# Kernel tuning notes

Measured on AMD Instinct MI355X. Metric: run time of the kernel, lower is better.

## Reference

```python
import jax, jax.numpy as jnp
import numpy as np

EMB_DIM = 1024
H = 16
HEAD_DIM = EMB_DIM // H
B = 2
S = 2048  # enc and dec seq len
LN_EPS = 1e-5


def setup_inputs() -> dict:
    key = jax.random.key(0)
    ks = jax.random.split(key, 8)
    scale_in = 1.0 / np.sqrt(EMB_DIM)
    scale_o = 1.0 / np.sqrt(H * HEAD_DIM)
    return {
        "enc_out": jax.random.normal(ks[0], (B, S, EMB_DIM), jnp.float32),
        "dec_out": jax.random.normal(ks[1], (B, S, EMB_DIM), jnp.float32),
        # stacked per-head projections, equivalent to h separate Linear(emb_dim, head_dim, bias=False)
        "Wq": jax.random.uniform(ks[2], (H, EMB_DIM, HEAD_DIM), jnp.float32, -scale_in, scale_in),
        "Wk": jax.random.uniform(ks[3], (H, EMB_DIM, HEAD_DIM), jnp.float32, -scale_in, scale_in),
        "Wv": jax.random.uniform(ks[4], (H, EMB_DIM, HEAD_DIM), jnp.float32, -scale_in, scale_in),
        "Wo": jax.random.uniform(ks[5], (H * HEAD_DIM, EMB_DIM), jnp.float32, -scale_o, scale_o),
        "gamma": jnp.ones((EMB_DIM,), jnp.float32),
        "beta": jnp.zeros((EMB_DIM,), jnp.float32),
    }


def reference(enc_out, dec_out, Wq, Wk, Wv, Wo, gamma, beta):
    d = Wq.shape[-1]
    # per-head projections, batched over heads (same math as the Python loop)
    q = jnp.einsum('bse,hed->bhsd', dec_out, Wq)   # queries from decoder
    k = jnp.einsum('bte,hed->bhtd', enc_out, Wk)   # keys from encoder
    v = jnp.einsum('bte,hed->bhtd', enc_out, Wv)   # values from encoder
    scores = jnp.einsum('bhsd,bhtd->bhst', q, k) / jnp.sqrt(jnp.asarray(d, q.dtype))
    att = jax.nn.softmax(scores, axis=-1)
    ctx = jnp.einsum('bhst,bhtd->bhsd', att, v)
    b, h, s, hd = ctx.shape
    ctx = ctx.transpose(0, 2, 1, 3).reshape(b, s, h * hd)  # concat heads along feature dim
    transformed = ctx @ Wo  # dropout is identity in eval mode
    x = dec_out + transformed
    mu = jnp.mean(x, axis=-1, keepdims=True)
    var = jnp.mean(jnp.square(x - mu), axis=-1, keepdims=True)
    return (x - mu) * jax.lax.rsqrt(var + LN_EPS) * gamma + beta
```

## Files before the change

### kernel.cpp

```cpp
#include <hip/hip_runtime.h>
#include <hip/hip_bf16.h>

#define EMB   1024
#define NH    16
#define HD    64
#define SEQ   2048
#define SA    72

typedef __attribute__((ext_vector_type(8))) short          bf16x8;
typedef __attribute__((ext_vector_type(8))) unsigned short us8;
typedef __attribute__((ext_vector_type(4))) float          f32x4;

__device__ __forceinline__ float u2f(unsigned short u) {
    return __uint_as_float(((unsigned)u) << 16);
}
__device__ __forceinline__ unsigned short f2u(float f) {
    __hip_bfloat16 b = __float2bfloat16(f);
    return *reinterpret_cast<unsigned short*>(&b);
}
__device__ __forceinline__ bool detect_bf16(const void* gamma) {
    return ((const unsigned short*)gamma)[0] == 0x3F80;
}
__device__ __forceinline__ f32x4 fzero() {
    f32x4 v; v.x = v.y = v.z = v.w = 0.f; return v;
}
__device__ __forceinline__ void ld16f(const void* p, size_t idx, bool isbf, float* o) {
    if (isbf) {
        const unsigned short* b = (const unsigned short*)p + idx;
        us8 v0 = *(const us8*)b, v1 = *(const us8*)(b + 8);
        #pragma unroll
        for (int i = 0; i < 8; ++i) { o[i] = u2f(v0[i]); o[8 + i] = u2f(v1[i]); }
    } else {
        const float* f = (const float*)p + idx;
        #pragma unroll
        for (int i = 0; i < 4; ++i) {
            float4 v = *(const float4*)(f + 4 * i);
            o[4*i] = v.x; o[4*i+1] = v.y; o[4*i+2] = v.z; o[4*i+3] = v.w;
        }
    }
}
__device__ __forceinline__ float ld1f(const void* p, size_t i, bool isbf) {
    return isbf ? u2f(((const unsigned short*)p)[i]) : ((const float*)p)[i];
}
__device__ __forceinline__ float4 ld4(const void* p, size_t idx, bool isbf) {
    if (isbf) {
        ushort4 t = *reinterpret_cast<const ushort4*>((const unsigned short*)p + idx);
        return make_float4(u2f(t.x), u2f(t.y), u2f(t.z), u2f(t.w));
    }
    return *reinterpret_cast<const float4*>((const float*)p + idx);
}
__device__ __forceinline__ us8 pk8(const float* s) {
    us8 v;
    #pragma unroll
    for (int i = 0; i < 8; ++i) v[i] = f2u(s[i]);
    return v;
}
__device__ __forceinline__ f32x4 mfma16(bf16x8 a, bf16x8 b, f32x4 c) {
    return __builtin_amdgcn_mfma_f32_16x16x32_bf16(a, b, c, 0, 0, 0);
}
__device__ __forceinline__ bf16x8 mk8(unsigned w0, unsigned w1, unsigned w2, unsigned w3) {
    union { unsigned u[4]; bf16x8 v; } x;
    x.u[0] = w0; x.u[1] = w1; x.u[2] = w2; x.u[3] = w3;
    return x.v;
}
__device__ __forceinline__ void gl_lds16(const unsigned short* g, unsigned short* l) {
    __builtin_amdgcn_global_load_lds(
        (const __attribute__((address_space(1))) void*)g,
        (__attribute__((address_space(3))) void*)l,
        16, 0, 0);
}

#define QSCALE 0.18033688f

__global__ __launch_bounds__(256) void convert_x_kernel(
    const void* __restrict__ dec, const void* __restrict__ enc,
    const void* __restrict__ gamma, unsigned short* __restrict__ xb)
{
    const bool isbf = detect_bf16(gamma);
    const size_t HALF = (size_t)4096 * 1024;
    size_t idx = ((size_t)blockIdx.x * 256 + threadIdx.x) * 16;
    const void* src; size_t off;
    if (idx < HALF) { src = dec; off = idx; } else { src = enc; off = idx - HALF; }
    float buf[16];
    ld16f(src, off, isbf, buf);
    *(us8*)&xb[idx]     = pk8(buf);
    *(us8*)&xb[idx + 8] = pk8(buf + 8);
}

__global__ __launch_bounds__(256) void transpose_w_kernel(
    const void* __restrict__ Wq, const void* __restrict__ Wk,
    const void* __restrict__ Wv, const void* __restrict__ gamma,
    unsigned short* __restrict__ wt)
{
    const bool isbf = detect_bf16(gamma);
    const int which = blockIdx.z, h = blockIdx.y, e0 = blockIdx.x * 64;
    const void* W = (which == 0) ? Wq : (which == 1 ? Wk : Wv);

    __shared__ unsigned short T[64][SA];
    const int sr = threadIdx.x >> 2, sc = (threadIdx.x & 3) * 16;

    float buf[16];
    ld16f(W, ((size_t)h * EMB + e0 + sr) * HD + sc, isbf, buf);
    #pragma unroll
    for (int i = 0; i < 16; ++i) T[sc + i][sr] = f2u(buf[i]);
    __syncthreads();
    us8 v0 = *(const us8*)&T[sr][sc];
    us8 v1 = *(const us8*)&T[sr][sc + 8];
    size_t o = (((size_t)which * NH + h) * HD + sr) * EMB + e0 + sc;
    *(us8*)&wt[o] = v0;
    *(us8*)&wt[o + 8] = v1;
}

__global__ __launch_bounds__(256) void transpose_wo_kernel(
    const void* __restrict__ Wo, const void* __restrict__ gamma,
    unsigned short* __restrict__ wot)
{
    const bool isbf = detect_bf16(gamma);
    const int n0 = blockIdx.x * 64, k0 = blockIdx.y * 64;
    __shared__ unsigned short T[64][SA];
    const int sr = threadIdx.x >> 2, sc = (threadIdx.x & 3) * 16;

    float buf[16];
    ld16f(Wo, (size_t)(k0 + sr) * EMB + n0 + sc, isbf, buf);
    #pragma unroll
    for (int i = 0; i < 16; ++i) T[sc + i][sr] = f2u(buf[i]);
    __syncthreads();
    us8 v0 = *(const us8*)&T[sr][sc];
    us8 v1 = *(const us8*)&T[sr][sc + 8];
    size_t o = (size_t)(n0 + sr) * EMB + k0 + sc;
    *(us8*)&wot[o] = v0;
    *(us8*)&wot[o + 8] = v1;
}

__global__ __launch_bounds__(256) void qkv_kernel(
    const unsigned short* __restrict__ xb,
    const unsigned short* __restrict__ wt,
    unsigned short* __restrict__ qo, unsigned short* __restrict__ ko,
    unsigned short* __restrict__ vt)
{
    const int id = blockIdx.x;
    const int xcd = id & 7, sl = id >> 3;
    const int m_t = xcd * 4 + (sl & 3);
    const int n_t = sl >> 2;
    const int m0 = m_t * 128, n0g = n_t * 128;
    const int which = n0g >> 10;
    const int nloc = n0g & 1023;
    const unsigned short* X = xb + ((which == 0) ? (size_t)0 : (size_t)4096 * 1024);

    __shared__ unsigned short smem[17408];
    unsigned short* const ldsA = smem;
    unsigned short* const ldsB = smem + 8192;

    const int tid = threadIdx.x, wv = tid >> 6, lane = tid & 63;
    const int lq = lane >> 4, lm = lane & 15;
    const int mw = (wv & 1) * 64, nw = (wv >> 1) * 64;

    const unsigned short* Wb = wt + (size_t)(which * 1024 + nloc) * EMB;

    const int seg0 = wv * 4;
    const int srow = lane >> 3;
    const int su   = (lane & 7) ^ srow;
    const unsigned short* aP[4];
    const unsigned short* bP[4];
    #pragma unroll
    for (int q = 0; q < 4; ++q) {
        const int s = seg0 + q;
        aP[q] = X  + (size_t)(m0 + 8 * s + srow) * EMB + su * 8;
        bP[q] = Wb + (size_t)(8 * s + srow) * EMB + su * 8;
    }

    f32x4 acc[4][4];
    #pragma unroll
    for (int i = 0; i < 4; ++i)
        #pragma unroll
        for (int j = 0; j < 4; ++j) acc[i][j] = fzero();

    const int xa = lm & 7;

    for (int k0 = 0; k0 < EMB; k0 += 64) {
        #pragma unroll
        for (int q = 0; q < 4; ++q) {
            gl_lds16(aP[q] + k0, ldsA + (seg0 + q) * 512);
            gl_lds16(bP[q] + k0, ldsB + (seg0 + q) * 512);
        }
        asm volatile("s_waitcnt vmcnt(0)" ::: "memory");
        __syncthreads();

        #pragma unroll
        for (int st = 0; st < 2; ++st) {
            const int u = (st * 4 + lq) ^ xa;
            bf16x8 af[4], bq[4];
            #pragma unroll
            for (int i = 0; i < 4; ++i)
                af[i] = *(const bf16x8*)(ldsA + (mw + i * 16 + lm) * 64 + u * 8);
            #pragma unroll
            for (int j = 0; j < 4; ++j)
                bq[j] = *(const bf16x8*)(ldsB + (nw + j * 16 + lm) * 64 + u * 8);
            #pragma unroll
            for (int i = 0; i < 4; ++i)
                #pragma unroll
                for (int j = 0; j < 4; ++j)
                    acc[i][j] = mfma16(af[i], bq[j], acc[i][j]);
        }
        __syncthreads();
    }

    const int b = m0 >> 11, s0 = m0 & (SEQ - 1);
    const float osc = (which == 0) ? QSCALE : 1.0f;
    if (which != 2) {
        unsigned short* Y = which ? ko : qo;
        #pragma unroll
        for (int i = 0; i < 4; ++i)
            #pragma unroll
            for (int j = 0; j < 4; ++j)
                #pragma unroll
                for (int r = 0; r < 4; ++r) {
                    int m = mw + i * 16 + lq * 4 + r;
                    int n = nloc + nw + j * 16 + lm;
                    int h = n >> 6, d = n & 63;
                    Y[(((size_t)b * NH + h) * SEQ + s0 + m) * HD + d] = f2u(acc[i][j][r] * osc);
                }
    } else {
        __syncthreads();
        unsigned short* vbuf = smem;
        #pragma unroll
        for (int i = 0; i < 4; ++i)
            #pragma unroll
            for (int j = 0; j < 4; ++j) {
                ushort4 p;
                p.x = f2u(acc[i][j][0]); p.y = f2u(acc[i][j][1]);
                p.z = f2u(acc[i][j][2]); p.w = f2u(acc[i][j][3]);
                *(ushort4*)&vbuf[(size_t)(nw + j * 16 + lm) * 136 + mw + i * 16 + lq * 4] = p;
            }
        __syncthreads();
        const int dd = tid >> 1, cc = (tid & 1) * 64;
        const int n = nloc + dd, h = n >> 6, d = n & 63;
        size_t o = (((size_t)b * NH + h) * HD + d) * SEQ + s0 + cc;
        #pragma unroll
        for (int jj = 0; jj < 8; ++jj)
            *(us8*)&vt[o + 8 * jj] = *(const us8*)&vbuf[(size_t)dd * 136 + cc + 8 * jj];
    }
}

__global__ __launch_bounds__(256) void attn_kernel(
    const unsigned short* __restrict__ qg,
    const unsigned short* __restrict__ kg,
    const unsigned short* __restrict__ vtg,
    unsigned short* __restrict__ ctx)
{
    __shared__ unsigned short Ks[2][64][SA];
    __shared__ unsigned short Vt[2][64][SA];

    const int tid = threadIdx.x, wv = tid >> 6, lane = tid & 63;
    const int lq = lane >> 4, lm = lane & 15;
    const int kr = tid >> 2, kc = (tid & 3) * 16;
    const int bh = blockIdx.x, q0 = blockIdx.y * 64;
    const unsigned short* Kg = kg + (size_t)bh * SEQ * HD;
    const unsigned short* Vg = vtg + (size_t)bh * HD * SEQ;

    bf16x8 qf[2];
    #pragma unroll
    for (int st = 0; st < 2; ++st)
        qf[st] = *(const bf16x8*)(qg + (size_t)bh * SEQ * HD
                      + (size_t)(q0 + wv * 16 + lm) * HD + st * 32 + lq * 8);

    bf16x8 onesf;
    #pragma unroll
    for (int i = 0; i < 8; ++i) onesf[i] = (short)0x3F80;

    f32x4 Of[4], lacc = fzero();
    #pragma unroll
    for (int t = 0; t < 4; ++t) Of[t] = fzero();

    us8 kreg0, kreg1, vreg0, vreg1;
    {
        const unsigned short* s1 = Kg + (size_t)kr * HD + kc;
        kreg0 = *(const us8*)s1; kreg1 = *(const us8*)(s1 + 8);
        const unsigned short* s2 = Vg + (size_t)kr * SEQ + kc;
        vreg0 = *(const us8*)s2; vreg1 = *(const us8*)(s2 + 8);
    }

    for (int it = 0; it < SEQ / 64; ++it) {
        const int cur = it & 1;
        *(us8*)&Ks[cur][kr][kc]     = kreg0;
        *(us8*)&Ks[cur][kr][kc + 8] = kreg1;
        *(us8*)&Vt[cur][kr][kc]     = vreg0;
        *(us8*)&Vt[cur][kr][kc + 8] = vreg1;
        __syncthreads();

        if (it + 1 < SEQ / 64) {
            const int t0 = (it + 1) * 64;
            const unsigned short* s1 = Kg + (size_t)(t0 + kr) * HD + kc;
            kreg0 = *(const us8*)s1; kreg1 = *(const us8*)(s1 + 8);
            const unsigned short* s2 = Vg + (size_t)kr * SEQ + t0 + kc;
            vreg0 = *(const us8*)s2; vreg1 = *(const us8*)(s2 + 8);
        }

        f32x4 sf[4];
        #pragma unroll
        for (int t = 0; t < 4; ++t) sf[t] = fzero();
        #pragma unroll
        for (int st = 0; st < 2; ++st)
            #pragma unroll
            for (int tt = 0; tt < 4; ++tt) {
                bf16x8 kf = *(const bf16x8*)&Ks[cur][lm + 16 * tt][st * 32 + lq * 8];
                sf[tt] = mfma16(kf, qf[st], sf[tt]);
            }

        unsigned pw[4][2];
        #pragma unroll
        for (int tt = 0; tt < 4; ++tt) {
            float p0 = exp2f(sf[tt][0]);
            float p1 = exp2f(sf[tt][1]);
            float p2 = exp2f(sf[tt][2]);
            float p3 = exp2f(sf[tt][3]);
            pw[tt][0] = (unsigned)f2u(p0) | ((unsigned)f2u(p1) << 16);
            pw[tt][1] = (unsigned)f2u(p2) | ((unsigned)f2u(p3) << 16);
        }
        #pragma unroll
        for (int a = 0; a < 2; ++a)
            #pragma unroll
            for (int c = 0; c < 2; ++c)
                asm("v_permlane32_swap_b32 %0, %1"
                    : "+v"(pw[2 * a][c]), "+v"(pw[2 * a + 1][c]));
        #pragma unroll
        for (int a = 0; a < 2; ++a)
            #pragma unroll
            for (int c = 0; c < 2; ++c)
                asm("v_permlane16_swap_b32 %0, %1"
                    : "+v"(pw[2 * a][c]), "+v"(pw[2 * a + 1][c]));

        #pragma unroll
        for (int st = 0; st < 2; ++st) {
            bf16x8 pf = mk8(pw[2 * st][0], pw[2 * st][1],
                            pw[2 * st + 1][0], pw[2 * st + 1][1]);
            #pragma unroll
            for (int t = 0; t < 4; ++t) {
                bf16x8 vf = *(const bf16x8*)&Vt[cur][lm + 16 * t][st * 32 + lq * 8];
                Of[t] = mfma16(pf, vf, Of[t]);
            }
            lacc = mfma16(pf, onesf, lacc);
        }
    }

    const int b = bh >> 4, h = bh & 15;
    #pragma unroll
    for (int r = 0; r < 4; ++r) {
        float inv = 1.0f / lacc[r];
        int srow = q0 + wv * 16 + lq * 4 + r;
        #pragma unroll
        for (int t = 0; t < 4; ++t) {
            int d = lm + 16 * t;
            ctx[((size_t)b * SEQ + srow) * EMB + h * HD + d] = f2u(Of[t][r] * inv);
        }
    }
}

__global__ __launch_bounds__(256) void oproj_kernel(
    const unsigned short* __restrict__ ctx,
    const unsigned short* __restrict__ wot,
    const void* __restrict__ dec, const void* __restrict__ gamma,
    float* __restrict__ x)
{
    const bool isbf = detect_bf16(gamma);
    const int id = blockIdx.x;
    const int xcd = id & 7, sl = id >> 3;
    const int m0 = (xcd * 4 + (sl & 3)) * 128;
    const int n0 = (sl >> 2) * 128;

    __shared__ unsigned short smem[16384];
    unsigned short* const ldsA = smem;
    unsigned short* const ldsB = smem + 8192;

    const int tid = threadIdx.x, wv = tid >> 6, lane = tid & 63;
    const int lq = lane >> 4, lm = lane & 15;
    const int mw = (wv & 1) * 64, nw = (wv >> 1) * 64;

    const int seg0 = wv * 4;
    const int srow = lane >> 3;
    const int su   = (lane & 7) ^ srow;
    const unsigned short* aP[4];
    const unsigned short* bP[4];
    #pragma unroll
    for (int q = 0; q < 4; ++q) {
        const int s = seg0 + q;
        aP[q] = ctx + (size_t)(m0 + 8 * s + srow) * EMB + su * 8;
        bP[q] = wot + (size_t)(n0 + 8 * s + srow) * EMB + su * 8;
    }

    f32x4 acc[4][4];
    #pragma unroll
    for (int i = 0; i < 4; ++i)
        #pragma unroll
        for (int j = 0; j < 4; ++j) acc[i][j] = fzero();

    const int xa = lm & 7;

    for (int k0 = 0; k0 < EMB; k0 += 64) {
        #pragma unroll
        for (int q = 0; q < 4; ++q) {
            gl_lds16(aP[q] + k0, ldsA + (seg0 + q) * 512);
            gl_lds16(bP[q] + k0, ldsB + (seg0 + q) * 512);
        }
        asm volatile("s_waitcnt vmcnt(0)" ::: "memory");
        __syncthreads();

        #pragma unroll
        for (int st = 0; st < 2; ++st) {
            const int u = (st * 4 + lq) ^ xa;
            bf16x8 af[4], bq[4];
            #pragma unroll
            for (int i = 0; i < 4; ++i)
                af[i] = *(const bf16x8*)(ldsA + (mw + i * 16 + lm) * 64 + u * 8);
            #pragma unroll
            for (int j = 0; j < 4; ++j)
                bq[j] = *(const bf16x8*)(ldsB + (nw + j * 16 + lm) * 64 + u * 8);
            #pragma unroll
            for (int i = 0; i < 4; ++i)
                #pragma unroll
                for (int j = 0; j < 4; ++j)
                    acc[i][j] = mfma16(af[i], bq[j], acc[i][j]);
        }
        __syncthreads();
    }

    #pragma unroll
    for (int i = 0; i < 4; ++i)
        #pragma unroll
        for (int j = 0; j < 4; ++j)
            #pragma unroll
            for (int r = 0; r < 4; ++r) {
                int m = m0 + mw + i * 16 + lq * 4 + r;
                int n = n0 + nw + j * 16 + lm;
                x[(size_t)m * EMB + n] = acc[i][j][r] + ld1f(dec, (size_t)m * EMB + n, isbf);
            }
}

__global__ __launch_bounds__(256) void ln_kernel(
    const float* __restrict__ x,
    const void* __restrict__ gamma,
    const void* __restrict__ beta,
    void* __restrict__ out)
{
    const bool isbf = detect_bf16(gamma);
    const int row = blockIdx.x;
    const int tid = threadIdx.x;
    const float* xr = x + (size_t)row * EMB;

    float4 xv = *reinterpret_cast<const float4*>(&xr[tid * 4]);
    float s1 = xv.x + xv.y + xv.z + xv.w;
    float s2 = xv.x * xv.x + xv.y * xv.y + xv.z * xv.z + xv.w * xv.w;

    #pragma unroll
    for (int off = 32; off > 0; off >>= 1) {
        s1 += __shfl_down(s1, off);
        s2 += __shfl_down(s2, off);
    }
    __shared__ float w1[4], w2[4];
    const int wid = tid >> 6, lane = tid & 63;
    if (lane == 0) { w1[wid] = s1; w2[wid] = s2; }
    __syncthreads();
    s1 = w1[0] + w1[1] + w1[2] + w1[3];
    s2 = w2[0] + w2[1] + w2[2] + w2[3];

    const float mu  = s1 * (1.0f / EMB);
    const float var = s2 * (1.0f / EMB) - mu * mu;
    const float rs  = rsqrtf(var + 1e-5f);

    float4 gv = ld4(gamma, (size_t)tid * 4, isbf);
    float4 bv = ld4(beta,  (size_t)tid * 4, isbf);
    float4 r;
    r.x = (xv.x - mu) * rs * gv.x + bv.x;
    r.y = (xv.y - mu) * rs * gv.y + bv.y;
    r.z = (xv.z - mu) * rs * gv.z + bv.z;
    r.w = (xv.w - mu) * rs * gv.w + bv.w;

    size_t o = (size_t)row * EMB + tid * 4;
    if (isbf) {
        ushort4 w;
        w.x = f2u(r.x); w.y = f2u(r.y); w.z = f2u(r.z); w.w = f2u(r.w);
        *reinterpret_cast<ushort4*>((unsigned short*)out + o) = w;
    } else {
        *reinterpret_cast<float4*>((float*)out + o) = r;
    }
}

extern "C" void kernel_launch(void* const* d_in, const int* in_sizes, int n_in,
                              void* d_out, int out_size, void* d_ws, size_t ws_size,
                              hipStream_t stream)
{
    const void* enc   = d_in[0];
    const void* dec   = d_in[1];
    const void* Wq    = d_in[2];
    const void* Wk    = d_in[3];
    const void* Wv    = d_in[4];
    const void* Wo    = d_in[5];
    const void* gamma = d_in[6];
    const void* beta  = d_in[7];

    char* w = (char*)d_ws;
    unsigned short* qws  = (unsigned short*)(w);
    unsigned short* kws  = (unsigned short*)(w + (size_t)8  * 1024 * 1024);
    unsigned short* vtws = (unsigned short*)(w + (size_t)16 * 1024 * 1024);
    unsigned short* wotw = (unsigned short*)(w + (size_t)16 * 1024 * 1024);
    unsigned short* wtws = (unsigned short*)(w + (size_t)24 * 1024 * 1024);
    unsigned short* cws  = (unsigned short*)(w + (size_t)24 * 1024 * 1024);
    float*          xws  = (float*)         (w);
    unsigned short* xbuf = (unsigned short*)d_out;

    convert_x_kernel   <<<2048,            256, 0, stream>>>(dec, enc, gamma, xbuf);
    transpose_w_kernel <<<dim3(16, 16, 3), 256, 0, stream>>>(Wq, Wk, Wv, gamma, wtws);
    qkv_kernel         <<<768,             256, 0, stream>>>(xbuf, wtws, qws, kws, vtws);
    attn_kernel        <<<dim3(32, 32),    256, 0, stream>>>(qws, kws, vtws, cws);
    transpose_wo_kernel<<<dim3(16, 16),    256, 0, stream>>>(Wo, gamma, wotw);
    oproj_kernel       <<<256,             256, 0, stream>>>(cws, wotw, dec, gamma, xws);
    ln_kernel          <<<4096,            256, 0, stream>>>(xws, gamma, beta, d_out);
}
```

Before: 258.7 us.

## Use direct global-to-LDS loads with XOR swizzle in attention kernel

Replaces the register-staged K/V prefetch in the attention kernel with direct global-to-LDS loads (gl_lds16) into double-buffered shared memory. Bank conflicts are avoided with an XOR swizzle instead of row padding. Explicit vmcnt waits plus a second barrier per iteration protect the buffers, and s_setprio raises wave priority around the MFMA sections. This removes VGPR staging and the LDS store instructions, at the cost of an extra barrier per tile and reliance on the helper's wait-count semantics.

Result: no change. 263.3 us (+1.8%).

```diff
diff --git a/kernel.cpp b/kernel.cpp
--- a/kernel.cpp
+++ b/kernel.cpp
@@ -248,16 +248,22 @@
     const unsigned short* __restrict__ vtg,
     unsigned short* __restrict__ ctx)
 {
-    __shared__ unsigned short Ks[2][64][SA];
-    __shared__ unsigned short Vt[2][64][SA];
+    __shared__ unsigned short Ks[2][4096];
+    __shared__ unsigned short Vt[2][4096];
 
     const int tid = threadIdx.x, wv = tid >> 6, lane = tid & 63;
     const int lq = lane >> 4, lm = lane & 15;
-    const int kr = tid >> 2, kc = (tid & 3) * 16;
     const int bh = blockIdx.x, q0 = blockIdx.y * 64;
     const unsigned short* Kg = kg + (size_t)bh * SEQ * HD;
     const unsigned short* Vg = vtg + (size_t)bh * HD * SEQ;
 
+    const int srow = lane >> 3;
+    const int su   = (lane & 7) ^ srow;
+    const unsigned short* kS0 = Kg + (size_t)(8 * wv       + srow) * HD  + su * 8;
+    const unsigned short* kS1 = Kg + (size_t)(8 * (wv + 4) + srow) * HD  + su * 8;
+    const unsigned short* vS0 = Vg + (size_t)(8 * wv       + srow) * SEQ + su * 8;
+    const unsigned short* vS1 = Vg + (size_t)(8 * (wv + 4) + srow) * SEQ + su * 8;
+
     bf16x8 qf[2];
     #pragma unroll
     for (int st = 0; st < 2; ++st)
@@ -272,40 +278,44 @@
     #pragma unroll
     for (int t = 0; t < 4; ++t) Of[t] = fzero();
 
-    us8 kreg0, kreg1, vreg0, vreg1;
+    const int xa = lm & 7;
+
     {
-        const unsigned short* s1 = Kg + (size_t)kr * HD + kc;
-        kreg0 = *(const us8*)s1; kreg1 = *(const us8*)(s1 + 8);
-        const unsigned short* s2 = Vg + (size_t)kr * SEQ + kc;
-        vreg0 = *(const us8*)s2; vreg1 = *(const us8*)(s2 + 8);
+        gl_lds16(kS0, &Ks[0][wv * 512]);
+        gl_lds16(kS1, &Ks[0][(wv + 4) * 512]);
+        gl_lds16(vS0, &Vt[0][wv * 512]);
+        gl_lds16(vS1, &Vt[0][(wv + 4) * 512]);
     }
 
     for (int it = 0; it < SEQ / 64; ++it) {
         const int cur = it & 1;
-        *(us8*)&Ks[cur][kr][kc]     = kreg0;
-        *(us8*)&Ks[cur][kr][kc + 8] = kreg1;
-        *(us8*)&Vt[cur][kr][kc]     = vreg0;
-        *(us8*)&Vt[cur][kr][kc + 8] = vreg1;
-        __syncthreads();
-
         if (it + 1 < SEQ / 64) {
-            const int t0 = (it + 1) * 64;
-            const unsigned short* s1 = Kg + (size_t)(t0 + kr) * HD + kc;
-            kreg0 = *(const us8*)s1; kreg1 = *(const us8*)(s1 + 8);
-            const unsigned short* s2 = Vg + (size_t)kr * SEQ + t0 + kc;
-            vreg0 = *(const us8*)s2; vreg1 = *(const us8*)(s2 + 8);
-        }
+            const size_t ko = (size_t)(it + 1) * 64 * HD;
+            const int    vo = (it + 1) * 64;
+            gl_lds16(kS0 + ko, &Ks[cur ^ 1][wv * 512]);
+            gl_lds16(kS1 + ko, &Ks[cur ^ 1][(wv + 4) * 512]);
+            gl_lds16(vS0 + vo, &Vt[cur ^ 1][wv * 512]);
+            gl_lds16(vS1 + vo, &Vt[cur ^ 1][(wv + 4) * 512]);
+            asm volatile("s_waitcnt vmcnt(4)" ::: "memory");
+        } else {
+            asm volatile("s_waitcnt vmcnt(0)" ::: "memory");
+        }
+        __syncthreads();
 
         f32x4 sf[4];
         #pragma unroll
         for (int t = 0; t < 4; ++t) sf[t] = fzero();
-        #pragma unroll
-        for (int st = 0; st < 2; ++st)
+        __builtin_amdgcn_s_setprio(1);
+        #pragma unroll
+        for (int st = 0; st < 2; ++st) {
+            const int u = (st * 4 + lq) ^ xa;
             #pragma unroll
             for (int tt = 0; tt < 4; ++tt) {
-                bf16x8 kf = *(const bf16x8*)&Ks[cur][lm + 16 * tt][st * 32 + lq * 8];
+                bf16x8 kf = *(const bf16x8*)&Ks[cur][(lm + 16 * tt) * 64 + u * 8];
                 sf[tt] = mfma16(kf, qf[st], sf[tt]);
             }
+        }
+        __builtin_amdgcn_s_setprio(0);
 
         unsigned pw[4][2];
         #pragma unroll
@@ -330,28 +340,32 @@
                 asm("v_permlane16_swap_b32 %0, %1"
                     : "+v"(pw[2 * a][c]), "+v"(pw[2 * a + 1][c]));
 
+        __builtin_amdgcn_s_setprio(1);
         #pragma unroll
         for (int st = 0; st < 2; ++st) {
+            const int u = (st * 4 + lq) ^ xa;
             bf16x8 pf = mk8(pw[2 * st][0], pw[2 * st][1],
                             pw[2 * st + 1][0], pw[2 * st + 1][1]);
             #pragma unroll
             for (int t = 0; t < 4; ++t) {
-                bf16x8 vf = *(const bf16x8*)&Vt[cur][lm + 16 * t][st * 32 + lq * 8];
+                bf16x8 vf = *(const bf16x8*)&Vt[cur][(lm + 16 * t) * 64 + u * 8];
                 Of[t] = mfma16(pf, vf, Of[t]);
             }
             lacc = mfma16(pf, onesf, lacc);
         }
+        __builtin_amdgcn_s_setprio(0);
+        __syncthreads();
     }
 
     const int b = bh >> 4, h = bh & 15;
     #pragma unroll
     for (int r = 0; r < 4; ++r) {
         float inv = 1.0f / lacc[r];
-        int srow = q0 + wv * 16 + lq * 4 + r;
+        int srow2 = q0 + wv * 16 + lq * 4 + r;
         #pragma unroll
         for (int t = 0; t < 4; ++t) {
             int d = lm + 16 * t;
-            ctx[((size_t)b * SEQ + srow) * EMB + h * HD + d] = f2u(Of[t][r] * inv);
+            ctx[((size_t)b * SEQ + srow2) * EMB + h * HD + d] = f2u(Of[t][r] * inv);
         }
     }
 }
```
